# Kernel tuning notes

Hardware: AMD Instinct MI355X
Metric: run time of the kernel (lower is better)

## Reference

```python
import jax, jax.numpy as jnp
import numpy as np

EPS = 1e-5

def layernorm(x, g, b):
    mu = jnp.mean(x, axis=-1, keepdims=True)
    var = jnp.var(x, axis=-1, keepdims=True)
    return (x - mu) / jnp.sqrt(var + EPS) * g + b

def hpmlp(x, wa, ba, wb, bb):
    # Linear(in,H) -> GELU(erf) -> Linear(H,H); dropout is identity in eval
    h = jax.nn.gelu(x @ wa + ba, approximate=False)
    return h @ wb + bb

def setup_inputs() -> dict:
    key = jax.random.key(0)
    ks = jax.random.split(key, 8)
    B, S, H = 16, 4096, 768
    s = 0.02
    return {
        "tokens": jax.random.normal(ks[0], (B, S + 1, H), jnp.float32),
        "lengths": jax.random.randint(ks[1], (B,), 1, S + 1),
        "q": jax.random.normal(ks[2], (2, H), jnp.float32) * s,
        "ln_g": jnp.ones((H,), jnp.float32),
        "ln_b": jnp.zeros((H,), jnp.float32),
        "w1a": jax.random.normal(ks[3], (3 * H, H), jnp.float32) * s,
        "b1a": jnp.zeros((H,), jnp.float32),
        "w1b": jax.random.normal(ks[4], (H, H), jnp.float32) * s,
        "b1b": jnp.zeros((H,), jnp.float32),
        "w2a": jax.random.normal(ks[5], (3 * H, H), jnp.float32) * s,
        "b2a": jnp.zeros((H,), jnp.float32),
        "w2b": jax.random.normal(ks[6], (H, H), jnp.float32) * s,
        "b2b": jnp.zeros((H,), jnp.float32),
    }

def reference(tokens, lengths, q, ln_g, ln_b, w1a, b1a, w1b, b1b, w2a, b2a, w2b, b2b):
    clf = tokens[:, 0]          # [B, H]
    x = tokens[:, 1:]           # [B, S, H]
    B, S, H = x.shape
    mask = jnp.arange(S)[None, :] < lengths[:, None]      # [B, S]
    m3 = mask[..., None]
    denom = lengths.astype(x.dtype)[:, None]
    mean_pooled = jnp.sum(jnp.where(m3, x, 0.0), axis=1) / denom
    max_pooled = jnp.max(jnp.where(m3, x, -jnp.inf), axis=1)
    min_pooled = jnp.min(jnp.where(m3, x, jnp.inf), axis=1)
    # PatchMerger with 2 learned queries over length-masked tokens
    xn = layernorm(x, ln_g, ln_b)                          # [B, S, H]
    logits = jnp.einsum("qh,bsh->bqs", q, xn) * (H ** -0.5)
    logits = jnp.where(mask[:, None, :], logits, -jnp.inf)
    attn = jax.nn.softmax(logits, axis=-1)                 # [B, 2, S]
    pmp = jnp.einsum("bqs,bsh->bqh", attn, xn)             # [B, 2, H]
    pooled_trad = jnp.concatenate([mean_pooled, max_pooled, min_pooled], -1)  # [B, 3H]
    pooled_learn = jnp.concatenate([pmp.reshape(B, 2 * H), clf], -1)          # [B, 3H]
    return jnp.concatenate([
        hpmlp(pooled_trad, w1a, b1a, w1b, b1b),
        hpmlp(pooled_learn, w2a, b2a, w2b, b2b),
    ], -1)
```

## Files before the change

kernel.cpp:

```cpp
#include <hip/hip_runtime.h>
#include <cmath>
#include <cstddef>

#define HD    768
#define BATCH 16
#define SROW  4097
#define NCH   64
#define CS    64
#define TPW   16
#define REC   3856
#define NK1   72
#define K1SEG 32
#define NK2   24
#define K2SEG 32
#define QSCALE 0.03608439182435161f

__device__ inline void wred4(float& a, float& b, float& c, float& d) {
#pragma unroll
  for (int off = 32; off > 0; off >>= 1) {
    a += __shfl_xor(a, off, 64);
    b += __shfl_xor(b, off, 64);
    c += __shfl_xor(c, off, 64);
    d += __shfl_xor(d, off, 64);
  }
}

__global__ __launch_bounds__(256, 3) void k1_pass(
    const float* __restrict__ tokens, const int* __restrict__ lengths,
    const float* __restrict__ q, const float* __restrict__ ln_g,
    const float* __restrict__ ln_b, float* __restrict__ rec)
{
  const int b = blockIdx.y, c = blockIdx.x;
  const int tid = threadIdx.x, w = tid >> 6, lane = tid & 63;
  const int len = lengths[b];
  if (c * CS >= len) return;

  float gq0[12], gq1[12];
  float G0 = 0.f, G1 = 0.f, C0 = 0.f, C1 = 0.f;
#pragma unroll
  for (int e = 0; e < 3; ++e) {
    const int off = e * 256 + lane * 4;
    const float4 qa = *(const float4*)(q + off);
    const float4 qb = *(const float4*)(q + HD + off);
    const float4 gg = *(const float4*)(ln_g + off);
    const float4 bb = *(const float4*)(ln_b + off);
    const float qav[4] = {qa.x, qa.y, qa.z, qa.w};
    const float qbv[4] = {qb.x, qb.y, qb.z, qb.w};
    const float ggv[4] = {gg.x, gg.y, gg.z, gg.w};
    const float bbv[4] = {bb.x, bb.y, bb.z, bb.w};
#pragma unroll
    for (int j = 0; j < 4; ++j) {
      const float g0 = ggv[j] * qav[j] * QSCALE;
      const float g1 = ggv[j] * qbv[j] * QSCALE;
      gq0[e * 4 + j] = g0;  gq1[e * 4 + j] = g1;
      G0 += g0;  G1 += g1;
      C0 = fmaf(bbv[j] * QSCALE, qav[j], C0);
      C1 = fmaf(bbv[j] * QSCALE, qbv[j], C1);
    }
  }
  wred4(G0, G1, C0, C1);

  float psum[12], pmax[12], pmin[12], A0[12], A1[12];
#pragma unroll
  for (int i = 0; i < 12; ++i) {
    psum[i] = 0.f; pmax[i] = -INFINITY; pmin[i] = INFINITY;
    A0[i] = 0.f; A1[i] = 0.f;
  }
  float m0 = -INFINITY, l0 = 0.f, B0 = 0.f;
  float m1 = -INFINITY, l1 = 0.f, B1 = 0.f;

  const int sbase = c * CS + w * TPW;
  const int rem0  = len - sbase;
  const int nt    = rem0 < 0 ? 0 : (rem0 < TPW ? rem0 : TPW);

  const float* xr = tokens + ((size_t)b * SROW + 1 + sbase) * HD + lane * 4;

  float4 nxa, nxb, nxc;
  if (nt > 0) {
    nxa = *(const float4*)(xr);
    nxb = *(const float4*)(xr + 256);
    nxc = *(const float4*)(xr + 512);
  }

  for (int t = 0; t < nt; ++t) {
    float xv[12];
    *(float4*)(xv)     = nxa;
    *(float4*)(xv + 4) = nxb;
    *(float4*)(xv + 8) = nxc;
    if (t + 1 < nt) {
      xr += HD;
      nxa = *(const float4*)(xr);
      nxb = *(const float4*)(xr + 256);
      nxc = *(const float4*)(xr + 512);
    }

    float s1 = 0.f, s2 = 0.f, dx0 = 0.f, dx1 = 0.f;
#pragma unroll
    for (int i = 0; i < 12; ++i) {
      s1 += xv[i];
      s2 = fmaf(xv[i], xv[i], s2);
      dx0 = fmaf(xv[i], gq0[i], dx0);
      dx1 = fmaf(xv[i], gq1[i], dx1);
    }
    wred4(s1, s2, dx0, dx1);
    const float mu   = s1 * (1.f / HD);
    const float var  = fmaf(-mu, mu, s2 * (1.f / HD));
    const float rstd = rsqrtf(var + 1e-5f);
    const float d0 = fmaf(rstd, fmaf(-mu, G0, dx0), C0);
    const float d1 = fmaf(rstd, fmaf(-mu, G1, dx1), C1);

    const float mn0 = fmaxf(m0, d0);
    const float al0 = __expf(m0 - mn0);
    const float p0  = __expf(d0 - mn0);
    const float c0  = p0 * rstd;
    l0 = fmaf(l0, al0, p0);  B0 = fmaf(B0, al0, c0 * mu);  m0 = mn0;

    const float mn1 = fmaxf(m1, d1);
    const float al1 = __expf(m1 - mn1);
    const float p1  = __expf(d1 - mn1);
    const float c1  = p1 * rstd;
    l1 = fmaf(l1, al1, p1);  B1 = fmaf(B1, al1, c1 * mu);  m1 = mn1;

#pragma unroll
    for (int i = 0; i < 12; ++i) {
      psum[i] += xv[i];
      pmax[i] = fmaxf(pmax[i], xv[i]);
      pmin[i] = fminf(pmin[i], xv[i]);
      A0[i] = fmaf(A0[i], al0, c0 * xv[i]);
      A1[i] = fmaf(A1[i], al1, c1 * xv[i]);
    }
  }

  __shared__ float ls[4][2][HD];
  __shared__ float lml[4][6];
#pragma unroll
  for (int e = 0; e < 3; ++e) {
    const int off = e * 256 + lane * 4;
    *(float4*)&ls[w][0][off] = *(const float4*)(psum + 4 * e);
    *(float4*)&ls[w][1][off] = *(const float4*)(pmax + 4 * e);
  }
  if (lane == 0) {
    lml[w][0] = m0; lml[w][1] = l0; lml[w][2] = B0;
    lml[w][3] = m1; lml[w][4] = l1; lml[w][5] = B1;
  }
  __syncthreads();

  float bm0 = -INFINITY, bm1 = -INFINITY;
#pragma unroll
  for (int wv = 0; wv < 4; ++wv) {
    bm0 = fmaxf(bm0, lml[wv][0]);
    bm1 = fmaxf(bm1, lml[wv][3]);
  }
  float sc0[4], sc1[4], bl0 = 0.f, bB0 = 0.f, bl1 = 0.f, bB1 = 0.f;
#pragma unroll
  for (int wv = 0; wv < 4; ++wv) {
    sc0[wv] = (lml[wv][1] > 0.f) ? __expf(lml[wv][0] - bm0) : 0.f;
    sc1[wv] = (lml[wv][4] > 0.f) ? __expf(lml[wv][3] - bm1) : 0.f;
    bl0 = fmaf(lml[wv][1], sc0[wv], bl0);  bB0 = fmaf(lml[wv][2], sc0[wv], bB0);
    bl1 = fmaf(lml[wv][4], sc1[wv], bl1);  bB1 = fmaf(lml[wv][5], sc1[wv], bB1);
  }

  float* r = rec + (size_t)(b * NCH + c) * REC;
#pragma unroll
  for (int e = 0; e < 3; ++e) {
    const int h = tid + 256 * e;
    float su = 0.f, mx = -INFINITY;
#pragma unroll
    for (int wv = 0; wv < 4; ++wv) {
      su += ls[wv][0][h];
      mx = fmaxf(mx, ls[wv][1][h]);
    }
    r[h] = su;  r[HD + h] = mx;
  }
  __syncthreads();
#pragma unroll
  for (int e = 0; e < 3; ++e) {
    const int off = e * 256 + lane * 4;
    *(float4*)&ls[w][0][off] = *(const float4*)(pmin + 4 * e);
    *(float4*)&ls[w][1][off] = *(const float4*)(A0 + 4 * e);
  }
  __syncthreads();
#pragma unroll
  for (int e = 0; e < 3; ++e) {
    const int h = tid + 256 * e;
    float mn_ = INFINITY, a0 = 0.f;
#pragma unroll
    for (int wv = 0; wv < 4; ++wv) {
      mn_ = fminf(mn_, ls[wv][0][h]);
      a0 = fmaf(ls[wv][1][h], sc0[wv], a0);
    }
    r[2 * HD + h] = mn_;  r[3 * HD + h] = a0;
  }
  __syncthreads();
#pragma unroll
  for (int e = 0; e < 3; ++e) {
    const int off = e * 256 + lane * 4;
    *(float4*)&ls[w][0][off] = *(const float4*)(A1 + 4 * e);
  }
  __syncthreads();
#pragma unroll
  for (int e = 0; e < 3; ++e) {
    const int h = tid + 256 * e;
    float a1 = 0.f;
#pragma unroll
    for (int wv = 0; wv < 4; ++wv) a1 = fmaf(ls[wv][0][h], sc1[wv], a1);
    r[4 * HD + h] = a1;
  }
  if (tid == 0) {
    r[3840] = bm0; r[3841] = bl0; r[3842] = bB0;
    r[3843] = bm1; r[3844] = bl1; r[3845] = bB1;
  }
}

__global__ __launch_bounds__(256) void k2_combine(
    const float* __restrict__ rec, const float* __restrict__ tokens,
    const int* __restrict__ lengths, const float* __restrict__ ln_g,
    const float* __restrict__ ln_b, const float* __restrict__ b1a,
    const float* __restrict__ b2a, const float* __restrict__ b1b,
    const float* __restrict__ b2b, float* __restrict__ pt,
    float* __restrict__ pl, float* __restrict__ hbuf,
    float* __restrict__ out)
{
  const int b = blockIdx.y, seg = blockIdx.x;
  const int tid = threadIdx.x, ln = tid & 63, cs = tid >> 6;
  const int h_ = seg * 64 + ln;
  const int len = lengths[b];
  const int nch = (len + CS - 1) / CS;
  const float* rb = rec + (size_t)b * NCH * REC;

  __shared__ float lmx[4][2];
  __shared__ float lsc[4][4];
  __shared__ float lbuf[5][4][64];

  float mq0 = -INFINITY, mq1 = -INFINITY;
  for (int cc = 0; cc < NCH / 4; ++cc) {
    const int c = cs * (NCH / 4) + cc;
    if (c >= nch) break;
    const float* rm = rb + (size_t)c * REC + 3840;
    mq0 = fmaxf(mq0, rm[0]);
    mq1 = fmaxf(mq1, rm[3]);
  }
  if (ln == 0) { lmx[cs][0] = mq0; lmx[cs][1] = mq1; }
  __syncthreads();
  const float mg0 = fmaxf(fmaxf(lmx[0][0], lmx[1][0]),
                          fmaxf(lmx[2][0], lmx[3][0]));
  const float mg1 = fmaxf(fmaxf(lmx[0][1], lmx[1][1]),
                          fmaxf(lmx[2][1], lmx[3][1]));

  float lg0 = 0.f, Bg0 = 0.f, lg1 = 0.f, Bg1 = 0.f;
  float S = 0.f, MX = -INFINITY, MN = INFINITY, A0 = 0.f, A1 = 0.f;
  for (int cc = 0; cc < NCH / 4; ++cc) {
    const int c = cs * (NCH / 4) + cc;
    if (c >= nch) break;
    const float* r = rb + (size_t)c * REC;
    const float e0 = __expf(r[3840] - mg0);
    const float e1 = __expf(r[3843] - mg1);
    lg0 = fmaf(r[3841], e0, lg0);  Bg0 = fmaf(r[3842], e0, Bg0);
    lg1 = fmaf(r[3844], e1, lg1);  Bg1 = fmaf(r[3845], e1, Bg1);
    S += r[h_];
    MX = fmaxf(MX, r[HD + h_]);
    MN = fminf(MN, r[2 * HD + h_]);
    A0 = fmaf(r[3 * HD + h_], e0, A0);
    A1 = fmaf(r[4 * HD + h_], e1, A1);
  }

  lbuf[0][cs][ln] = S;  lbuf[1][cs][ln] = MX; lbuf[2][cs][ln] = MN;
  lbuf[3][cs][ln] = A0; lbuf[4][cs][ln] = A1;
  if (ln == 0) {
    lsc[cs][0] = lg0; lsc[cs][1] = Bg0; lsc[cs][2] = lg1; lsc[cs][3] = Bg1;
  }
  __syncthreads();
  if (cs == 0) {
#pragma unroll
    for (int k = 1; k < 4; ++k) {
      S  += lbuf[0][k][ln];
      MX  = fmaxf(MX, lbuf[1][k][ln]);
      MN  = fminf(MN, lbuf[2][k][ln]);
      A0 += lbuf[3][k][ln];
      A1 += lbuf[4][k][ln];
    }
    const float Lg0 = lsc[0][0] + lsc[1][0] + lsc[2][0] + lsc[3][0];
    const float BG0 = lsc[0][1] + lsc[1][1] + lsc[2][1] + lsc[3][1];
    const float Lg1 = lsc[0][2] + lsc[1][2] + lsc[2][2] + lsc[3][2];
    const float BG1 = lsc[0][3] + lsc[1][3] + lsc[2][3] + lsc[3][3];
    const float invlen = 1.f / (float)len;
    const float il0 = 1.f / Lg0, il1 = 1.f / Lg1;
    const float gg = ln_g[h_], bb = ln_b[h_];
    float* ptb = pt + (size_t)b * 2304;
    float* plb = pl + (size_t)b * 2304;
    ptb[h_] = S * invlen;
    ptb[HD + h_] = MX;
    ptb[2 * HD + h_] = MN;
    plb[h_]      = fmaf(gg, (A0 - BG0) * il0, bb);
    plb[HD + h_] = fmaf(gg, (A1 - BG1) * il1, bb);
    plb[2 * HD + h_] = tokens[(size_t)b * SROW * HD + h_];
  }

  const int gidx = (b * 12 + seg) * 256 + tid;
  if (gidx < 2 * BATCH * HD) {
    const int j = gidx % HD, r2 = (gidx / HD) & 1;
    out[gidx] = (r2 ? b2b : b1b)[j];
  } else {
    const int g2 = gidx - 2 * BATCH * HD;
    const int j = g2 % HD;
    const int mlp = g2 / (BATCH * HD);
    hbuf[g2] = (mlp ? b2a : b1a)[j];
  }
}

__global__ __launch_bounds__(256) void k3_gemm1(
    const float* __restrict__ pt, const float* __restrict__ pl,
    const float* __restrict__ w1a, const float* __restrict__ w2a,
    float* __restrict__ hbuf)
{
  const int kseg = blockIdx.x, jseg = blockIdx.y, mlp = blockIdx.z;
  const int j = jseg * 256 + threadIdx.x;
  const float* xs = mlp ? pl : pt;
  const float* wA = mlp ? w2a : w1a;
  const int k0 = kseg * K1SEG;

  float wv[K1SEG];
#pragma unroll
  for (int kk = 0; kk < K1SEG; ++kk)
    wv[kk] = wA[(size_t)(k0 + kk) * HD + j];

  float acc[16];
#pragma unroll
  for (int bb = 0; bb < 16; ++bb) {
    const float4* xp = (const float4*)(xs + bb * 2304 + k0);
    float a = 0.f;
#pragma unroll
    for (int qq = 0; qq < K1SEG / 4; ++qq) {
      const float4 xq = xp[qq];
      a = fmaf(xq.x, wv[4 * qq + 0], a);
      a = fmaf(xq.y, wv[4 * qq + 1], a);
      a = fmaf(xq.z, wv[4 * qq + 2], a);
      a = fmaf(xq.w, wv[4 * qq + 3], a);
    }
    acc[bb] = a;
  }

  float* hm = hbuf + (size_t)mlp * BATCH * HD;
#pragma unroll
  for (int bb = 0; bb < 16; ++bb)
    unsafeAtomicAdd(&hm[bb * HD + j], acc[bb]);
}

__global__ __launch_bounds__(256) void k4_gemm2(
    const float* __restrict__ hbuf, const float* __restrict__ w1b,
    const float* __restrict__ w2b, float* __restrict__ out)
{
  const int kseg = blockIdx.x, jseg = blockIdx.y, mlp = blockIdx.z;
  const int tid = threadIdx.x;
  const int j = jseg * 256 + tid;
  const int k0 = kseg * K2SEG;
  __shared__ float hs[16][K2SEG];

  const float* wB = mlp ? w2b : w1b;
  float wv[K2SEG];
#pragma unroll
  for (int kk = 0; kk < K2SEG; ++kk)
    wv[kk] = wB[(size_t)(k0 + kk) * HD + j];

  const float* hm = hbuf + (size_t)mlp * BATCH * HD;
#pragma unroll
  for (int u = 0; u < (16 * K2SEG) / 256; ++u) {
    const int lin = tid + 256 * u;
    const int bb = lin / K2SEG, kk = lin % K2SEG;
    const float a = hm[bb * HD + k0 + kk];
    hs[bb][kk] = 0.5f * a * (1.f + erff(a * 0.70710678118654752f));
  }
  __syncthreads();

  float acc2[16];
#pragma unroll
  for (int bb = 0; bb < 16; ++bb) {
    float a = 0.f;
#pragma unroll
    for (int kk = 0; kk < K2SEG; ++kk)
      a = fmaf(hs[bb][kk], wv[kk], a);
    acc2[bb] = a;
  }
#pragma unroll
  for (int bb = 0; bb < 16; ++bb)
    unsafeAtomicAdd(&out[(size_t)bb * 1536 + mlp * HD + j], acc2[bb]);
}

extern "C" void kernel_launch(void* const* d_in, const int* in_sizes, int n_in,
                              void* d_out, int out_size, void* d_ws, size_t ws_size,
                              hipStream_t stream)
{
  const float* tokens = (const float*)d_in[0];
  const int*   lengths = (const int*)d_in[1];
  const float* q    = (const float*)d_in[2];
  const float* ln_g = (const float*)d_in[3];
  const float* ln_b = (const float*)d_in[4];
  const float* w1a  = (const float*)d_in[5];
  const float* b1a  = (const float*)d_in[6];
  const float* w1b  = (const float*)d_in[7];
  const float* b1b  = (const float*)d_in[8];
  const float* w2a  = (const float*)d_in[9];
  const float* b2a  = (const float*)d_in[10];
  const float* w2b  = (const float*)d_in[11];
  const float* b2b  = (const float*)d_in[12];
  float* out = (float*)d_out;

  float* ws   = (float*)d_ws;
  float* rec  = ws;
  float* pt   = rec + (size_t)BATCH * NCH * REC;
  float* pl   = pt + (size_t)BATCH * 2304;
  float* hbuf = pl + (size_t)BATCH * 2304;

  hipLaunchKernelGGL(k1_pass, dim3(NCH, BATCH), dim3(256), 0, stream,
                     tokens, lengths, q, ln_g, ln_b, rec);
  hipLaunchKernelGGL(k2_combine, dim3(12, BATCH), dim3(256), 0, stream,
                     rec, tokens, lengths, ln_g, ln_b, b1a, b2a, b1b, b2b,
                     pt, pl, hbuf, out);
  hipLaunchKernelGGL(k3_gemm1, dim3(NK1, 3, 2), dim3(256), 0, stream,
                     pt, pl, w1a, w2a, hbuf);
  hipLaunchKernelGGL(k4_gemm2, dim3(NK2, 3, 2), dim3(256), 0, stream,
                     hbuf, w1b, w2b, out);
}
```

Measured before the change: 311.4 us.

## Replace per-chunk records and combine kernel with global atomic accumulation

The pass kernel now merges its per-chunk statistics straight into a small per-batch accumulator using global atomics. Sums use float atomic add, and max/min use integer atomics on an order-preserving key encoding of the float. The separate combine kernel is removed, and its finalisation (mean division, the LayerNorm affine step, softmax normalisation) moves into the GEMM1 shared-memory prologue. A small init kernel now seeds the accumulators and the bias buffers. The online-softmax running max is dropped in favour of a plain exp(logit) sum: this cuts exp work and avoids writing and reading the large record buffer, but it could overflow if the logits are large.

```diff
diff --git a/kernel.cpp b/kernel.cpp
--- a/kernel.cpp
+++ b/kernel.cpp
@@ -8,13 +8,25 @@
 #define NCH   64
 #define CS    64
 #define TPW   16
-#define REC   3856
 #define NK1   72
 #define K1SEG 32
 #define NK2   24
 #define K2SEG 32
 #define QSCALE 0.03608439182435161f
 
+#define ACCSTR 3848
+#define KOFF 0x007FFFFFu
+
+__device__ inline unsigned fkey(float f) {
+  int i = __float_as_int(f);
+  return (i < 0) ? ~(unsigned)i : ((unsigned)i | 0x80000000u);
+}
+__device__ inline float fdec(unsigned s) {
+  unsigned u = s + KOFF;
+  int i = (u & 0x80000000u) ? (int)(u & 0x7FFFFFFFu) : ~(int)u;
+  return __int_as_float(i);
+}
+
 __device__ inline void wred4(float& a, float& b, float& c, float& d) {
 #pragma unroll
   for (int off = 32; off > 0; off >>= 1) {
@@ -25,10 +37,33 @@
   }
 }
 
+__global__ __launch_bounds__(256) void k0_init(
+    const float* __restrict__ b1a, const float* __restrict__ b2a,
+    const float* __restrict__ b1b, const float* __restrict__ b2b,
+    float* __restrict__ acc, float* __restrict__ hbuf,
+    float* __restrict__ out)
+{
+  const int g = blockIdx.x * 256 + threadIdx.x;
+  const int NACC = BATCH * ACCSTR;
+  const int NH   = 2 * BATCH * HD;
+  if (g < NACC) {
+    const int o = g % ACCSTR;
+    ((unsigned*)acc)[g] = (o >= 3072 && o < 3840) ? 0xFFFFFFFFu : 0u;
+  } else if (g < NACC + NH) {
+    const int g2 = g - NACC;
+    const int j = g2 % HD, mlp = g2 / (BATCH * HD);
+    hbuf[g2] = (mlp ? b2a : b1a)[j];
+  } else if (g < NACC + NH + BATCH * 2 * HD) {
+    const int g3 = g - NACC - NH;
+    const int j = g3 % HD, mlp = (g3 / HD) & 1;
+    out[g3] = (mlp ? b2b : b1b)[j];
+  }
+}
+
 __global__ __launch_bounds__(256, 3) void k1_pass(
     const float* __restrict__ tokens, const int* __restrict__ lengths,
     const float* __restrict__ q, const float* __restrict__ ln_g,
-    const float* __restrict__ ln_b, float* __restrict__ rec)
+    const float* __restrict__ ln_b, float* __restrict__ acc)
 {
   const int b = blockIdx.y, c = blockIdx.x;
   const int tid = threadIdx.x, w = tid >> 6, lane = tid & 63;
@@ -66,8 +101,7 @@
     psum[i] = 0.f; pmax[i] = -INFINITY; pmin[i] = INFINITY;
     A0[i] = 0.f; A1[i] = 0.f;
   }
-  float m0 = -INFINITY, l0 = 0.f, B0 = 0.f;
-  float m1 = -INFINITY, l1 = 0.f, B1 = 0.f;
+  float l0 = 0.f, B0 = 0.f, l1 = 0.f, B1 = 0.f;
 
   const int sbase = c * CS + w * TPW;
   const int rem0  = len - sbase;
@@ -109,241 +143,148 @@
     const float d0 = fmaf(rstd, fmaf(-mu, G0, dx0), C0);
     const float d1 = fmaf(rstd, fmaf(-mu, G1, dx1), C1);
 
-    const float mn0 = fmaxf(m0, d0);
-    const float al0 = __expf(m0 - mn0);
-    const float p0  = __expf(d0 - mn0);
-    const float c0  = p0 * rstd;
-    l0 = fmaf(l0, al0, p0);  B0 = fmaf(B0, al0, c0 * mu);  m0 = mn0;
-
-    const float mn1 = fmaxf(m1, d1);
-    const float al1 = __expf(m1 - mn1);
-    const float p1  = __expf(d1 - mn1);
-    const float c1  = p1 * rstd;
-    l1 = fmaf(l1, al1, p1);  B1 = fmaf(B1, al1, c1 * mu);  m1 = mn1;
+    const float p0 = __expf(d0);
+    const float c0 = p0 * rstd;
+    l0 += p0;  B0 = fmaf(c0, mu, B0);
+
+    const float p1 = __expf(d1);
+    const float c1 = p1 * rstd;
+    l1 += p1;  B1 = fmaf(c1, mu, B1);
 
 #pragma unroll
     for (int i = 0; i < 12; ++i) {
       psum[i] += xv[i];
       pmax[i] = fmaxf(pmax[i], xv[i]);
       pmin[i] = fminf(pmin[i], xv[i]);
-      A0[i] = fmaf(A0[i], al0, c0 * xv[i]);
-      A1[i] = fmaf(A1[i], al1, c1 * xv[i]);
-    }
-  }
-
-  __shared__ float ls[4][2][HD];
-  __shared__ float lml[4][6];
+      A0[i] = fmaf(c0, xv[i], A0[i]);
+      A1[i] = fmaf(c1, xv[i], A1[i]);
+    }
+  }
+
+  __shared__ float ls[4][3][HD];
+  __shared__ float lml[4][4];
+  float* ab = acc + (size_t)b * ACCSTR;
+  unsigned* abu = (unsigned*)ab;
+
 #pragma unroll
   for (int e = 0; e < 3; ++e) {
     const int off = e * 256 + lane * 4;
     *(float4*)&ls[w][0][off] = *(const float4*)(psum + 4 * e);
     *(float4*)&ls[w][1][off] = *(const float4*)(pmax + 4 * e);
+    *(float4*)&ls[w][2][off] = *(const float4*)(pmin + 4 * e);
   }
   if (lane == 0) {
-    lml[w][0] = m0; lml[w][1] = l0; lml[w][2] = B0;
-    lml[w][3] = m1; lml[w][4] = l1; lml[w][5] = B1;
-  }
-  __syncthreads();
-
-  float bm0 = -INFINITY, bm1 = -INFINITY;
-#pragma unroll
-  for (int wv = 0; wv < 4; ++wv) {
-    bm0 = fmaxf(bm0, lml[wv][0]);
-    bm1 = fmaxf(bm1, lml[wv][3]);
-  }
-  float sc0[4], sc1[4], bl0 = 0.f, bB0 = 0.f, bl1 = 0.f, bB1 = 0.f;
-#pragma unroll
-  for (int wv = 0; wv < 4; ++wv) {
-    sc0[wv] = (lml[wv][1] > 0.f) ? __expf(lml[wv][0] - bm0) : 0.f;
-    sc1[wv] = (lml[wv][4] > 0.f) ? __expf(lml[wv][3] - bm1) : 0.f;
-    bl0 = fmaf(lml[wv][1], sc0[wv], bl0);  bB0 = fmaf(lml[wv][2], sc0[wv], bB0);
-    bl1 = fmaf(lml[wv][4], sc1[wv], bl1);  bB1 = fmaf(lml[wv][5], sc1[wv], bB1);
-  }
-
-  float* r = rec + (size_t)(b * NCH + c) * REC;
+    lml[w][0] = l0; lml[w][1] = B0; lml[w][2] = l1; lml[w][3] = B1;
+  }
+  __syncthreads();
 #pragma unroll
   for (int e = 0; e < 3; ++e) {
     const int h = tid + 256 * e;
-    float su = 0.f, mx = -INFINITY;
+    float su = 0.f, mx = -INFINITY, mn = INFINITY;
 #pragma unroll
     for (int wv = 0; wv < 4; ++wv) {
       su += ls[wv][0][h];
       mx = fmaxf(mx, ls[wv][1][h]);
-    }
-    r[h] = su;  r[HD + h] = mx;
-  }
-  __syncthreads();
+      mn = fminf(mn, ls[wv][2][h]);
+    }
+    unsafeAtomicAdd(&ab[h], su);
+    atomicMax(&abu[2304 + h], fkey(mx) - KOFF);
+    atomicMin(&abu[3072 + h], fkey(mn) - KOFF);
+  }
+  __syncthreads();
+
 #pragma unroll
   for (int e = 0; e < 3; ++e) {
     const int off = e * 256 + lane * 4;
-    *(float4*)&ls[w][0][off] = *(const float4*)(pmin + 4 * e);
-    *(float4*)&ls[w][1][off] = *(const float4*)(A0 + 4 * e);
+    *(float4*)&ls[w][0][off] = *(const float4*)(A0 + 4 * e);
+    *(float4*)&ls[w][1][off] = *(const float4*)(A1 + 4 * e);
   }
   __syncthreads();
 #pragma unroll
   for (int e = 0; e < 3; ++e) {
     const int h = tid + 256 * e;
-    float mn_ = INFINITY, a0 = 0.f;
+    float a0 = 0.f, a1 = 0.f;
 #pragma unroll
     for (int wv = 0; wv < 4; ++wv) {
-      mn_ = fminf(mn_, ls[wv][0][h]);
-      a0 = fmaf(ls[wv][1][h], sc0[wv], a0);
-    }
-    r[2 * HD + h] = mn_;  r[3 * HD + h] = a0;
-  }
-  __syncthreads();
-#pragma unroll
-  for (int e = 0; e < 3; ++e) {
-    const int off = e * 256 + lane * 4;
-    *(float4*)&ls[w][0][off] = *(const float4*)(A1 + 4 * e);
-  }
-  __syncthreads();
-#pragma unroll
-  for (int e = 0; e < 3; ++e) {
-    const int h = tid + 256 * e;
-    float a1 = 0.f;
-#pragma unroll
-    for (int wv = 0; wv < 4; ++wv) a1 = fmaf(ls[wv][0][h], sc1[wv], a1);
-    r[4 * HD + h] = a1;
+      a0 += ls[wv][0][h];
+      a1 += ls[wv][1][h];
+    }
+    unsafeAtomicAdd(&ab[768 + h], a0);
+    unsafeAtomicAdd(&ab[1536 + h], a1);
   }
   if (tid == 0) {
-    r[3840] = bm0; r[3841] = bl0; r[3842] = bB0;
-    r[3843] = bm1; r[3844] = bl1; r[3845] = bB1;
-  }
-}
-
-__global__ __launch_bounds__(256) void k2_combine(
-    const float* __restrict__ rec, const float* __restrict__ tokens,
+    float L0 = 0.f, Bb0 = 0.f, L1 = 0.f, Bb1 = 0.f;
+#pragma unroll
+    for (int wv = 0; wv < 4; ++wv) {
+      L0 += lml[wv][0]; Bb0 += lml[wv][1];
+      L1 += lml[wv][2]; Bb1 += lml[wv][3];
+    }
+    unsafeAtomicAdd(&ab[3840], L0);
+    unsafeAtomicAdd(&ab[3841], Bb0);
+    unsafeAtomicAdd(&ab[3842], L1);
+    unsafeAtomicAdd(&ab[3843], Bb1);
+  }
+}
+
+__global__ __launch_bounds__(256) void k3_gemm1(
+    const float* __restrict__ acc, const float* __restrict__ tokens,
     const int* __restrict__ lengths, const float* __restrict__ ln_g,
-    const float* __restrict__ ln_b, const float* __restrict__ b1a,
-    const float* __restrict__ b2a, const float* __restrict__ b1b,
-    const float* __restrict__ b2b, float* __restrict__ pt,
-    float* __restrict__ pl, float* __restrict__ hbuf,
-    float* __restrict__ out)
-{
-  const int b = blockIdx.y, seg = blockIdx.x;
-  const int tid = threadIdx.x, ln = tid & 63, cs = tid >> 6;
-  const int h_ = seg * 64 + ln;
-  const int len = lengths[b];
-  const int nch = (len + CS - 1) / CS;
-  const float* rb = rec + (size_t)b * NCH * REC;
-
-  __shared__ float lmx[4][2];
-  __shared__ float lsc[4][4];
-  __shared__ float lbuf[5][4][64];
-
-  float mq0 = -INFINITY, mq1 = -INFINITY;
-  for (int cc = 0; cc < NCH / 4; ++cc) {
-    const int c = cs * (NCH / 4) + cc;
-    if (c >= nch) break;
-    const float* rm = rb + (size_t)c * REC + 3840;
-    mq0 = fmaxf(mq0, rm[0]);
-    mq1 = fmaxf(mq1, rm[3]);
-  }
-  if (ln == 0) { lmx[cs][0] = mq0; lmx[cs][1] = mq1; }
-  __syncthreads();
-  const float mg0 = fmaxf(fmaxf(lmx[0][0], lmx[1][0]),
-                          fmaxf(lmx[2][0], lmx[3][0]));
-  const float mg1 = fmaxf(fmaxf(lmx[0][1], lmx[1][1]),
-                          fmaxf(lmx[2][1], lmx[3][1]));
-
-  float lg0 = 0.f, Bg0 = 0.f, lg1 = 0.f, Bg1 = 0.f;
-  float S = 0.f, MX = -INFINITY, MN = INFINITY, A0 = 0.f, A1 = 0.f;
-  for (int cc = 0; cc < NCH / 4; ++cc) {
-    const int c = cs * (NCH / 4) + cc;
-    if (c >= nch) break;
-    const float* r = rb + (size_t)c * REC;
-    const float e0 = __expf(r[3840] - mg0);
-    const float e1 = __expf(r[3843] - mg1);
-    lg0 = fmaf(r[3841], e0, lg0);  Bg0 = fmaf(r[3842], e0, Bg0);
-    lg1 = fmaf(r[3844], e1, lg1);  Bg1 = fmaf(r[3845], e1, Bg1);
-    S += r[h_];
-    MX = fmaxf(MX, r[HD + h_]);
-    MN = fminf(MN, r[2 * HD + h_]);
-    A0 = fmaf(r[3 * HD + h_], e0, A0);
-    A1 = fmaf(r[4 * HD + h_], e1, A1);
-  }
-
-  lbuf[0][cs][ln] = S;  lbuf[1][cs][ln] = MX; lbuf[2][cs][ln] = MN;
-  lbuf[3][cs][ln] = A0; lbuf[4][cs][ln] = A1;
-  if (ln == 0) {
-    lsc[cs][0] = lg0; lsc[cs][1] = Bg0; lsc[cs][2] = lg1; lsc[cs][3] = Bg1;
-  }
-  __syncthreads();
-  if (cs == 0) {
-#pragma unroll
-    for (int k = 1; k < 4; ++k) {
-      S  += lbuf[0][k][ln];
-      MX  = fmaxf(MX, lbuf[1][k][ln]);
-      MN  = fminf(MN, lbuf[2][k][ln]);
-      A0 += lbuf[3][k][ln];
-      A1 += lbuf[4][k][ln];
-    }
-    const float Lg0 = lsc[0][0] + lsc[1][0] + lsc[2][0] + lsc[3][0];
-    const float BG0 = lsc[0][1] + lsc[1][1] + lsc[2][1] + lsc[3][1];
-    const float Lg1 = lsc[0][2] + lsc[1][2] + lsc[2][2] + lsc[3][2];
-    const float BG1 = lsc[0][3] + lsc[1][3] + lsc[2][3] + lsc[3][3];
-    const float invlen = 1.f / (float)len;
-    const float il0 = 1.f / Lg0, il1 = 1.f / Lg1;
-    const float gg = ln_g[h_], bb = ln_b[h_];
-    float* ptb = pt + (size_t)b * 2304;
-    float* plb = pl + (size_t)b * 2304;
-    ptb[h_] = S * invlen;
-    ptb[HD + h_] = MX;
-    ptb[2 * HD + h_] = MN;
-    plb[h_]      = fmaf(gg, (A0 - BG0) * il0, bb);
-    plb[HD + h_] = fmaf(gg, (A1 - BG1) * il1, bb);
-    plb[2 * HD + h_] = tokens[(size_t)b * SROW * HD + h_];
-  }
-
-  const int gidx = (b * 12 + seg) * 256 + tid;
-  if (gidx < 2 * BATCH * HD) {
-    const int j = gidx % HD, r2 = (gidx / HD) & 1;
-    out[gidx] = (r2 ? b2b : b1b)[j];
-  } else {
-    const int g2 = gidx - 2 * BATCH * HD;
-    const int j = g2 % HD;
-    const int mlp = g2 / (BATCH * HD);
-    hbuf[g2] = (mlp ? b2a : b1a)[j];
-  }
-}
-
-__global__ __launch_bounds__(256) void k3_gemm1(
-    const float* __restrict__ pt, const float* __restrict__ pl,
-    const float* __restrict__ w1a, const float* __restrict__ w2a,
-    float* __restrict__ hbuf)
+    const float* __restrict__ ln_b, const float* __restrict__ w1a,
+    const float* __restrict__ w2a, float* __restrict__ hbuf)
 {
   const int kseg = blockIdx.x, jseg = blockIdx.y, mlp = blockIdx.z;
-  const int j = jseg * 256 + threadIdx.x;
-  const float* xs = mlp ? pl : pt;
+  const int tid = threadIdx.x;
+  const int j = jseg * 256 + tid;
+  const int k0 = kseg * K1SEG;
+  __shared__ float xls[16][K1SEG];
+
+#pragma unroll
+  for (int u = 0; u < 2; ++u) {
+    const int lin = tid + 256 * u;
+    const int bb = lin >> 5, kk = lin & 31;
+    const int k = k0 + kk;
+    const float* ab = acc + (size_t)bb * ACCSTR;
+    const unsigned* abu = (const unsigned*)ab;
+    float v;
+    if (!mlp) {
+      if (k < 768)            v = ab[k] / (float)lengths[bb];
+      else if (k < 1536)      v = fdec(abu[2304 + (k - 768)]);
+      else                    v = fdec(abu[3072 + (k - 1536)]);
+    } else {
+      if (k < 1536) {
+        const int qi = (k >= 768);
+        const int h = qi ? (k - 768) : k;
+        const float A = ab[768 + qi * 768 + h];
+        const float l = ab[3840 + 2 * qi], Bs = ab[3841 + 2 * qi];
+        v = fmaf(ln_g[h], (A - Bs) / l, ln_b[h]);
+      } else {
+        v = tokens[(size_t)bb * SROW * HD + (k - 1536)];
+      }
+    }
+    xls[bb][kk] = v;
+  }
+  __syncthreads();
+
   const float* wA = mlp ? w2a : w1a;
-  const int k0 = kseg * K1SEG;
-
   float wv[K1SEG];
 #pragma unroll
   for (int kk = 0; kk < K1SEG; ++kk)
     wv[kk] = wA[(size_t)(k0 + kk) * HD + j];
 
-  float acc[16];
+  float acc2[16];
 #pragma unroll
   for (int bb = 0; bb < 16; ++bb) {
-    const float4* xp = (const float4*)(xs + bb * 2304 + k0);
     float a = 0.f;
 #pragma unroll
-    for (int qq = 0; qq < K1SEG / 4; ++qq) {
-      const float4 xq = xp[qq];
-      a = fmaf(xq.x, wv[4 * qq + 0], a);
-      a = fmaf(xq.y, wv[4 * qq + 1], a);
-      a = fmaf(xq.z, wv[4 * qq + 2], a);
-      a = fmaf(xq.w, wv[4 * qq + 3], a);
-    }
-    acc[bb] = a;
+    for (int kk = 0; kk < K1SEG; ++kk)
+      a = fmaf(xls[bb][kk], wv[kk], a);
+    acc2[bb] = a;
   }
 
   float* hm = hbuf + (size_t)mlp * BATCH * HD;
 #pragma unroll
   for (int bb = 0; bb < 16; ++bb)
-    unsafeAtomicAdd(&hm[bb * HD + j], acc[bb]);
+    unsafeAtomicAdd(&hm[bb * HD + j], acc2[bb]);
 }
 
 __global__ __launch_bounds__(256) void k4_gemm2(
@@ -406,18 +347,16 @@
   float* out = (float*)d_out;
 
   float* ws   = (float*)d_ws;
-  float* rec  = ws;
-  float* pt   = rec + (size_t)BATCH * NCH * REC;
-  float* pl   = pt + (size_t)BATCH * 2304;
-  float* hbuf = pl + (size_t)BATCH * 2304;
-
+  float* acc  = ws;
+  float* hbuf = acc + (size_t)BATCH * ACCSTR;
+
+  const int ninit = BATCH * ACCSTR + 2 * BATCH * HD + BATCH * 2 * HD;
+  hipLaunchKernelGGL(k0_init, dim3((ninit + 255) / 256), dim3(256), 0, stream,
+                     b1a, b2a, b1b, b2b, acc, hbuf, out);
   hipLaunchKernelGGL(k1_pass, dim3(NCH, BATCH), dim3(256), 0, stream,
-                     tokens, lengths, q, ln_g, ln_b, rec);
-  hipLaunchKernelGGL(k2_combine, dim3(12, BATCH), dim3(256), 0, stream,
-                     rec, tokens, lengths, ln_g, ln_b, b1a, b2a, b1b, b2b,
-                     pt, pl, hbuf, out);
+                     tokens, lengths, q, ln_g, ln_b, acc);
   hipLaunchKernelGGL(k3_gemm1, dim3(NK1, 3, 2), dim3(256), 0, stream,
-                     pt, pl, w1a, w2a, hbuf);
+                     acc, tokens, lengths, ln_g, ln_b, w1a, w2a, hbuf);
   hipLaunchKernelGGL(k4_gemm2, dim3(NK2, 3, 2), dim3(256), 0, stream,
                      hbuf, w1b, w2b, out);
 }
```

New measurement: 294.4 us. -5.5%, faster.
